# Kernel tuning notes

Measured on AMD Instinct MI355X. Metric: run time of the kernel, lower is better.

## Reference

```python
import jax, jax.numpy as jnp
import numpy as np

H = 2048      # hidden_size
F = 1408      # moe_intermediate_size
E = 8         # num_experts
K = 2         # num_activated_experts
B, S = 4, 1024


def setup_inputs() -> dict:
    key = jax.random.key(0)
    ks = jax.random.split(key, 9)
    sc = 0.02
    return {
        "hidden_states": jax.random.normal(ks[0], (B, S, H), dtype=jnp.float32),
        "gate_w": jax.random.normal(ks[1], (E, H), dtype=jnp.float32) * sc,
        "bias": jnp.zeros((E,), dtype=jnp.float32),
        # shared expert (num_shared_experts = 1); torch Linear weight layout [out, in]
        "ws1": jax.random.normal(ks[2], (F, H), dtype=jnp.float32) * sc,
        "ws2": jax.random.normal(ks[3], (H, F), dtype=jnp.float32) * sc,
        "ws3": jax.random.normal(ks[4], (F, H), dtype=jnp.float32) * sc,
        # routed experts stacked along leading E axis
        "we1": jax.random.normal(ks[5], (E, F, H), dtype=jnp.float32) * sc,
        "we2": jax.random.normal(ks[6], (E, H, F), dtype=jnp.float32) * sc,
        "we3": jax.random.normal(ks[7], (E, F, H), dtype=jnp.float32) * sc,
    }


def reference(hidden_states, gate_w, bias, ws1, ws2, ws3, we1, we2, we3):
    orig_shape = hidden_states.shape
    x = hidden_states.reshape(-1, orig_shape[-1])      # [T, H]
    T = x.shape[0]

    # shared expert (SwiGLU)
    shared = (jax.nn.silu(x @ ws1.T) * (x @ ws3.T)) @ ws2.T   # [T, H]

    # sigmoid gating with bias-adjusted top-k selection
    scores = jax.nn.sigmoid(x @ gate_w.T)              # [T, E]
    routing_scores = scores + bias
    _, topk_idx = jax.lax.top_k(routing_scores, K)     # [T, K]
    sel = jnp.take_along_axis(scores, topk_idx, axis=1)
    gates = sel / sel.sum(axis=-1, keepdims=True)      # [T, K]

    # dense combine weights c[t, e] (top-k indices are distinct per token)
    c = jnp.zeros((T, E), dtype=x.dtype).at[jnp.arange(T)[:, None], topk_idx].add(gates)

    # all-expert SwiGLU, combined with sparse gate weights
    h1 = jnp.einsum("th,efh->etf", x, we1)             # [E, T, F]
    h3 = jnp.einsum("th,efh->etf", x, we3)
    act = jax.nn.silu(h1) * h3
    routed = jnp.einsum("etf,ehf,te->th", act, we2, c) # [T, H]

    return (shared + routed).reshape(orig_shape)
```

## Files before the change

### kernel.cpp

```cpp
#include <hip/hip_runtime.h>
#include <cstdint>
#include <cstddef>

#define TDIM 4096
#define HDIM 2048
#define FDIM 1408
#define NEXP 8
#define NSLOT (TDIM * 2)
#define BK 32

typedef _Float16 half8 __attribute__((ext_vector_type(8)));
typedef _Float16 half4 __attribute__((ext_vector_type(4)));
typedef float floatx4 __attribute__((ext_vector_type(4)));

#define AS1 __attribute__((address_space(1)))
#define AS3 __attribute__((address_space(3)))

__device__ __forceinline__ void g2l16(const _Float16* g, _Float16* l) {
  __builtin_amdgcn_global_load_lds((const AS1 unsigned*)g, (AS3 unsigned*)l, 16, 0, 0);
}

static constexpr size_t ws_align(size_t x) { return (x + 511) & ~(size_t)511; }
static constexpr size_t WS_XB     = 0;
static constexpr size_t WS_ACT_S  = WS_XB    + (size_t)TDIM * HDIM * 2;
static constexpr size_t WS_ACT_R  = WS_ACT_S + (size_t)TDIM * FDIM * 2;
static constexpr size_t WS_TOKE   = WS_ACT_R + (size_t)NSLOT * FDIM * 2;
static constexpr size_t WS_TOKG   = WS_TOKE  + (size_t)TDIM * 2 * 4;
static constexpr size_t WS_SLOTT  = WS_TOKG  + (size_t)TDIM * 2 * 4;
static constexpr size_t WS_SLOTG  = WS_SLOTT + (size_t)NSLOT * 4;
static constexpr size_t WS_TOKS   = WS_SLOTG + (size_t)NSLOT * 4;
static constexpr size_t WS_COUNTS = WS_TOKS  + (size_t)TDIM * 2 * 4;
static constexpr size_t WS_FILL   = WS_COUNTS + 64;
static constexpr size_t WS_OFFS   = WS_FILL   + 64;
static constexpr size_t WS_WS1H   = ws_align(WS_OFFS + 64);
static constexpr size_t WS_WS3H   = WS_WS1H + (size_t)FDIM * HDIM * 2;
static constexpr size_t WS_WS2H   = WS_WS3H + (size_t)FDIM * HDIM * 2;
static constexpr size_t WS_WE1H   = WS_WS2H + (size_t)HDIM * FDIM * 2;
static constexpr size_t WS_WE3H   = WS_WE1H + (size_t)NEXP * FDIM * HDIM * 2;
static constexpr size_t WS_WE2H   = WS_WE3H + (size_t)NEXP * FDIM * HDIM * 2;
static constexpr size_t WS_H1S    = WS_WE2H + (size_t)NEXP * HDIM * FDIM * 2;
static constexpr size_t WS_H1R    = WS_H1S + (size_t)TDIM * FDIM * 2;
static constexpr size_t WS_RB     = WS_H1R + (size_t)NSLOT * FDIM * 2;
static constexpr size_t WS_END    = WS_RB + (size_t)NSLOT * HDIM * 2;


__global__ void zero_meta_kernel(int* __restrict__ counts) {
  if (threadIdx.x < 32) counts[threadIdx.x] = 0;
}

__global__ void cvt3_kernel(const float* __restrict__ s0, const float* __restrict__ s1,
                            const float* __restrict__ s2, _Float16* __restrict__ d0,
                            _Float16* __restrict__ d1, _Float16* __restrict__ d2) {
  const float* s;
  _Float16* d;
  if (blockIdx.y == 0)      { s = s0; d = d0; }
  else if (blockIdx.y == 1) { s = s1; d = d1; }
  else                      { s = s2; d = d2; }
  size_t i = ((size_t)blockIdx.x * 256 + threadIdx.x) * 8;
  float4 a = *(const float4*)(s + i);
  float4 b = *(const float4*)(s + i + 4);
  half8 h;
  h[0] = (_Float16)a.x; h[1] = (_Float16)a.y; h[2] = (_Float16)a.z; h[3] = (_Float16)a.w;
  h[4] = (_Float16)b.x; h[5] = (_Float16)b.y; h[6] = (_Float16)b.z; h[7] = (_Float16)b.w;
  *(half8*)(d + i) = h;
}

__global__ void gate_kernel(const float* __restrict__ x, const float* __restrict__ gw,
                            const float* __restrict__ bias, _Float16* __restrict__ xb,
                            int* __restrict__ toke, float* __restrict__ tokg,
                            int* __restrict__ counts) {
  const int wid  = blockIdx.x * 4 + (threadIdx.x >> 6);
  const int lane = threadIdx.x & 63;
  const float4* xv = (const float4*)(x + (size_t)wid * HDIM);
  const float4* gv = (const float4*)gw;
  _Float16* xrow = xb + (size_t)wid * HDIM;
  float acc[NEXP];
#pragma unroll
  for (int e = 0; e < NEXP; ++e) acc[e] = 0.f;
#pragma unroll
  for (int i = 0; i < 8; ++i) {
    float4 xq = xv[lane + 64 * i];
    half4 hq;
    hq[0] = (_Float16)xq.x; hq[1] = (_Float16)xq.y;
    hq[2] = (_Float16)xq.z; hq[3] = (_Float16)xq.w;
    *(half4*)(xrow + 4 * (lane + 64 * i)) = hq;
#pragma unroll
    for (int e = 0; e < NEXP; ++e) {
      float4 gq = gv[e * 512 + lane + 64 * i];
      acc[e] += xq.x * gq.x + xq.y * gq.y + xq.z * gq.z + xq.w * gq.w;
    }
  }
#pragma unroll
  for (int e = 0; e < NEXP; ++e) {
    float v = acc[e];
    for (int off = 32; off; off >>= 1) v += __shfl_xor(v, off);
    acc[e] = v;
  }
  if (lane == 0) {
    float s[NEXP], r[NEXP];
#pragma unroll
    for (int e = 0; e < NEXP; ++e) {
      s[e] = 1.f / (1.f + __expf(-acc[e]));
      r[e] = s[e] + bias[e];
    }
    int e0 = 0;
#pragma unroll
    for (int e = 1; e < NEXP; ++e) if (r[e] > r[e0]) e0 = e;
    int e1 = -1;
#pragma unroll
    for (int e = 0; e < NEXP; ++e) if (e != e0 && (e1 < 0 || r[e] > r[e1])) e1 = e;
    float g0 = s[e0], g1 = s[e1];
    float inv = 1.f / (g0 + g1);
    toke[wid * 2]     = e0;
    toke[wid * 2 + 1] = e1;
    tokg[wid * 2]     = g0 * inv;
    tokg[wid * 2 + 1] = g1 * inv;
    atomicAdd(&counts[e0], 1);
    atomicAdd(&counts[e1], 1);
  }
}

__global__ void offsets_kernel(const int* __restrict__ counts, int* __restrict__ offs) {
  if (threadIdx.x == 0) {
    int o = 0;
    for (int e = 0; e < NEXP; ++e) { offs[e] = o; o += counts[e]; }
  }
}

__global__ void scatter_kernel(const int* __restrict__ toke, const float* __restrict__ tokg,
                               const int* __restrict__ offs, int* __restrict__ fill,
                               int* __restrict__ slott, float* __restrict__ slotg,
                               int* __restrict__ tokslot) {
  int t = blockIdx.x * 256 + threadIdx.x;
#pragma unroll
  for (int j = 0; j < 2; ++j) {
    int e = toke[t * 2 + j];
    float g = tokg[t * 2 + j];
    int p = offs[e] + atomicAdd(&fill[e], 1);
    slott[p] = t;
    slotg[p] = g;
    tokslot[t * 2 + j] = p;
  }
}


template <bool FIN>
__global__ __launch_bounds__(256) void up_gemm(
    const _Float16* __restrict__ xb,
    const _Float16* __restrict__ wsh, const _Float16* __restrict__ weh,
    _Float16* __restrict__ dsts, _Float16* __restrict__ dstr,
    const _Float16* __restrict__ h1s, const _Float16* __restrict__ h1r,
    const int* __restrict__ counts, const int* __restrict__ offs,
    const int* __restrict__ slott) {
  constexpr int GX = FDIM / 128;
  constexpr int GY = TDIM / 128;
  const int orig = blockIdx.x + GX * (blockIdx.y + GY * blockIdx.z);
  const int k8 = orig & 7, s = orig >> 3;
  const int g = k8 + 8 * (s / GX);
  const int lid = g * GX + (s % GX);
  const int bx = lid % GX;
  const int by = (lid / GX) % GY;
  const int bz = lid / (GX * GY);

  int cnt = TDIM, base = 0;
  const _Float16* __restrict__ W = wsh;
  _Float16* __restrict__ dst = dsts;
  const _Float16* __restrict__ h1 = h1s;
  bool gather = false;
  if (bz > 0) {
    const int e = bz - 1;
    cnt = counts[e];
    base = offs[e];
    if ((int)(by * 128) >= cnt) return;
    W = weh + (size_t)e * FDIM * HDIM;
    dst = dstr;
    h1 = h1r;
    gather = true;
  }
  const int m0 = by * 128, n0 = bx * 128;

  __shared__ _Float16 As[2][128 * BK];
  __shared__ _Float16 Bs[2][128 * BK];

  const int tid = threadIdx.x, lane = tid & 63, wv = tid >> 6;
  const int wm = wv >> 1, wn = wv & 1;
  const int lrow = lane & 15, quad = lane >> 4;

  const _Float16 *srcA[2], *srcB[2];
#pragma unroll
  for (int j = 0; j < 2; ++j) {
    const int rr = wv * 32 + j * 16 + (lane >> 2);
    const int gc = ((lane & 3) ^ ((rr >> 1) & 3)) * 8;
    const int m = m0 + rr;
    int tok;
    if (gather) tok = slott[base + (m < cnt ? m : cnt - 1)];
    else tok = m;
    srcA[j] = xb + (size_t)tok * HDIM + gc;
    srcB[j] = W + (size_t)(n0 + rr) * HDIM + gc;
  }

  floatx4 acc[4][4] = {};
  const int cA = (quad ^ ((lrow >> 1) & 3)) * 8;

#pragma unroll
  for (int j = 0; j < 2; ++j) {
    const int lb = (wv * 32 + j * 16) * BK;
    g2l16(srcA[j], &As[0][lb]);
    g2l16(srcB[j], &Bs[0][lb]);
  }
  __syncthreads();

  for (int t = 0; t < HDIM / BK; ++t) {
    const int cur = t & 1;
    if (t + 1 < HDIM / BK) {
      const int k0 = (t + 1) * BK;
#pragma unroll
      for (int j = 0; j < 2; ++j) {
        const int lb = (wv * 32 + j * 16) * BK;
        g2l16(srcA[j] + k0, &As[cur ^ 1][lb]);
        g2l16(srcB[j] + k0, &Bs[cur ^ 1][lb]);
      }
    }
    half8 af[4], bf[4];
#pragma unroll
    for (int i = 0; i < 4; ++i)
      af[i] = *(const half8*)&As[cur][(wm * 64 + i * 16 + lrow) * BK + cA];
#pragma unroll
    for (int i = 0; i < 4; ++i)
      bf[i] = *(const half8*)&Bs[cur][(wn * 64 + i * 16 + lrow) * BK + cA];
#pragma unroll
    for (int ms = 0; ms < 4; ++ms)
#pragma unroll
      for (int ns = 0; ns < 4; ++ns)
        acc[ms][ns] = __builtin_amdgcn_mfma_f32_16x16x32_f16(af[ms], bf[ns], acc[ms][ns], 0, 0, 0);
    __syncthreads();
  }

#pragma unroll
  for (int ms = 0; ms < 4; ++ms)
#pragma unroll
    for (int ns = 0; ns < 4; ++ns)
#pragma unroll
      for (int r = 0; r < 4; ++r) {
        const int rl = wm * 64 + ms * 16 + quad * 4 + r;
        const int f = n0 + wn * 64 + ns * 16 + lrow;
        const int m = m0 + rl;
        if (gather && m >= cnt) continue;
        const size_t row = gather ? (size_t)(base + m) : (size_t)m;
        float v = acc[ms][ns][r];
        if constexpr (FIN) {
          float h = (float)h1[row * FDIM + f];
          float a = h / (1.f + __expf(-h)) * v;
          dst[row * FDIM + f] = (_Float16)a;
        } else {
          dst[row * FDIM + f] = (_Float16)v;
        }
      }
}

__global__ __launch_bounds__(256) void down_kernel(
    const _Float16* __restrict__ acts, const _Float16* __restrict__ actr,
    const _Float16* __restrict__ ws2h, const _Float16* __restrict__ we2h,
    float* __restrict__ out, _Float16* __restrict__ rbuf,
    const int* __restrict__ counts, const int* __restrict__ offs) {
  constexpr int GX = HDIM / 128;
  constexpr int GY = TDIM / 128;
  const int orig = blockIdx.x + GX * (blockIdx.y + GY * blockIdx.z);
  const int k8 = orig & 7, s = orig >> 3;
  const int g = k8 + 8 * (s / GX);
  const int lid = g * GX + (s % GX);
  const int bx = lid % GX;
  const int by = (lid / GX) % GY;
  const int bz = lid / (GX * GY);

  int cnt = TDIM, base = 0;
  const _Float16* __restrict__ A = acts;
  const _Float16* __restrict__ W = ws2h;
  bool gather = false;
  if (bz > 0) {
    const int e = bz - 1;
    cnt = counts[e];
    base = offs[e];
    if ((int)(by * 128) >= cnt) return;
    A = actr;
    W = we2h + (size_t)e * HDIM * FDIM;
    gather = true;
  }
  const int m0 = by * 128, n0 = bx * 128;

  __shared__ _Float16 As[2][128 * BK];
  __shared__ _Float16 Bs[2][128 * BK];

  const int tid = threadIdx.x, lane = tid & 63, wv = tid >> 6;
  const int wm = wv >> 1, wn = wv & 1;
  const int lrow = lane & 15, quad = lane >> 4;

  const _Float16 *srcA[2], *srcB[2];
#pragma unroll
  for (int j = 0; j < 2; ++j) {
    const int rr = wv * 32 + j * 16 + (lane >> 2);
    const int gc = ((lane & 3) ^ ((rr >> 1) & 3)) * 8;
    const int m = m0 + rr;
    int srow;
    if (gather) srow = base + (m < cnt ? m : cnt - 1);
    else srow = m;
    srcA[j] = A + (size_t)srow * FDIM + gc;
    srcB[j] = W + (size_t)(n0 + rr) * FDIM + gc;
  }

  floatx4 acc[4][4] = {};
  const int cA = (quad ^ ((lrow >> 1) & 3)) * 8;

#pragma unroll
  for (int j = 0; j < 2; ++j) {
    const int lb = (wv * 32 + j * 16) * BK;
    g2l16(srcA[j], &As[0][lb]);
    g2l16(srcB[j], &Bs[0][lb]);
  }
  __syncthreads();

  for (int t = 0; t < FDIM / BK; ++t) {
    const int cur = t & 1;
    if (t + 1 < FDIM / BK) {
      const int k0 = (t + 1) * BK;
#pragma unroll
      for (int j = 0; j < 2; ++j) {
        const int lb = (wv * 32 + j * 16) * BK;
        g2l16(srcA[j] + k0, &As[cur ^ 1][lb]);
        g2l16(srcB[j] + k0, &Bs[cur ^ 1][lb]);
      }
    }
    half8 af[4], bf[4];
#pragma unroll
    for (int i = 0; i < 4; ++i)
      af[i] = *(const half8*)&As[cur][(wm * 64 + i * 16 + lrow) * BK + cA];
#pragma unroll
    for (int i = 0; i < 4; ++i)
      bf[i] = *(const half8*)&Bs[cur][(wn * 64 + i * 16 + lrow) * BK + cA];
#pragma unroll
    for (int ms = 0; ms < 4; ++ms)
#pragma unroll
      for (int ns = 0; ns < 4; ++ns)
        acc[ms][ns] = __builtin_amdgcn_mfma_f32_16x16x32_f16(af[ms], bf[ns], acc[ms][ns], 0, 0, 0);
    __syncthreads();
  }

#pragma unroll
  for (int ms = 0; ms < 4; ++ms)
#pragma unroll
    for (int ns = 0; ns < 4; ++ns)
#pragma unroll
      for (int r = 0; r < 4; ++r) {
        float v = acc[ms][ns][r];
        const int rl = wm * 64 + ms * 16 + quad * 4 + r;
        const int h = n0 + wn * 64 + ns * 16 + lrow;
        const int m = m0 + rl;
        if (gather) {
          if (m < cnt) rbuf[(size_t)(base + m) * HDIM + h] = (_Float16)v;
        } else {
          out[(size_t)m * HDIM + h] = v;
        }
      }
}

__global__ void merge_kernel(float* __restrict__ out, const _Float16* __restrict__ rbuf,
                             const int* __restrict__ tokslot, const float* __restrict__ tokg) {
  const int t = blockIdx.x;
  const int hc = threadIdx.x * 8;
  const int p0 = tokslot[t * 2], p1 = tokslot[t * 2 + 1];
  const float g0 = tokg[t * 2], g1 = tokg[t * 2 + 1];
  half8 r0 = *(const half8*)(rbuf + (size_t)p0 * HDIM + hc);
  half8 r1 = *(const half8*)(rbuf + (size_t)p1 * HDIM + hc);
  float* o = out + (size_t)t * HDIM + hc;
  float4 a = *(float4*)o;
  float4 b = *(float4*)(o + 4);
  a.x += g0 * (float)r0[0] + g1 * (float)r1[0];
  a.y += g0 * (float)r0[1] + g1 * (float)r1[1];
  a.z += g0 * (float)r0[2] + g1 * (float)r1[2];
  a.w += g0 * (float)r0[3] + g1 * (float)r1[3];
  b.x += g0 * (float)r0[4] + g1 * (float)r1[4];
  b.y += g0 * (float)r0[5] + g1 * (float)r1[5];
  b.z += g0 * (float)r0[6] + g1 * (float)r1[6];
  b.w += g0 * (float)r0[7] + g1 * (float)r1[7];
  *(float4*)o = a;
  *(float4*)(o + 4) = b;
}


extern "C" void kernel_launch(void* const* d_in, const int* in_sizes, int n_in,
                              void* d_out, int out_size, void* d_ws, size_t ws_size,
                              hipStream_t stream) {
  const float* x    = (const float*)d_in[0];
  const float* gw   = (const float*)d_in[1];
  const float* bias = (const float*)d_in[2];
  const float* ws1  = (const float*)d_in[3];
  const float* ws2  = (const float*)d_in[4];
  const float* ws3  = (const float*)d_in[5];
  const float* we1  = (const float*)d_in[6];
  const float* we2  = (const float*)d_in[7];
  const float* we3  = (const float*)d_in[8];
  float* out = (float*)d_out;

  char* ws = (char*)d_ws;
  _Float16* xb   = (_Float16*)(ws + WS_XB);
  _Float16* acts = (_Float16*)(ws + WS_ACT_S);
  _Float16* actr = (_Float16*)(ws + WS_ACT_R);
  int*   toke  = (int*)(ws + WS_TOKE);
  float* tokg  = (float*)(ws + WS_TOKG);
  int*   slott = (int*)(ws + WS_SLOTT);
  float* slotg = (float*)(ws + WS_SLOTG);
  int*   toks  = (int*)(ws + WS_TOKS);
  int* counts  = (int*)(ws + WS_COUNTS);
  int* fill    = (int*)(ws + WS_FILL);
  int* offs    = (int*)(ws + WS_OFFS);
  _Float16* ws1h = (_Float16*)(ws + WS_WS1H);
  _Float16* ws3h = (_Float16*)(ws + WS_WS3H);
  _Float16* ws2h = (_Float16*)(ws + WS_WS2H);
  _Float16* we1h = (_Float16*)(ws + WS_WE1H);
  _Float16* we3h = (_Float16*)(ws + WS_WE3H);
  _Float16* we2h = (_Float16*)(ws + WS_WE2H);
  _Float16* h1s  = (_Float16*)(ws + WS_H1S);
  _Float16* h1r  = (_Float16*)(ws + WS_H1R);
  _Float16* rbuf = (_Float16*)(ws + WS_RB);

  hipLaunchKernelGGL(zero_meta_kernel, dim3(1), dim3(64), 0, stream, counts);
  hipLaunchKernelGGL(gate_kernel, dim3(1024), dim3(256), 0, stream, x, gw, bias, xb, toke, tokg, counts);
  hipLaunchKernelGGL(offsets_kernel, dim3(1), dim3(64), 0, stream, counts, offs);
  hipLaunchKernelGGL(scatter_kernel, dim3(16), dim3(256), 0, stream, toke, tokg, offs, fill, slott, slotg, toks);

  constexpr int GS = (FDIM * HDIM) / 2048;
  constexpr int GR = (NEXP * FDIM * HDIM) / 2048;
  hipLaunchKernelGGL(cvt3_kernel, dim3(GS, 3), dim3(256), 0, stream, ws1, ws3, ws2, ws1h, ws3h, ws2h);
  hipLaunchKernelGGL(cvt3_kernel, dim3(GR, 3), dim3(256), 0, stream, we1, we3, we2, we1h, we3h, we2h);

  hipLaunchKernelGGL((up_gemm<false>), dim3(FDIM / 128, TDIM / 128, NEXP + 1), dim3(256), 0, stream,
                     xb, ws1h, we1h, h1s, h1r, nullptr, nullptr, counts, offs, slott);
  hipLaunchKernelGGL((up_gemm<true>), dim3(FDIM / 128, TDIM / 128, NEXP + 1), dim3(256), 0, stream,
                     xb, ws3h, we3h, acts, actr, h1s, h1r, counts, offs, slott);
  hipLaunchKernelGGL(down_kernel, dim3(HDIM / 128, TDIM / 128, NEXP + 1), dim3(256), 0, stream,
                     acts, actr, ws2h, we2h, out, rbuf, counts, offs);
  hipLaunchKernelGGL(merge_kernel, dim3(TDIM), dim3(256), 0, stream, out, rbuf, toks, tokg);
}
```

Before: 912.8 us.

## Double K-tile depth and drop LDS double buffering in expert GEMMs

Raises the K tile from 32 to 64 in both expert GEMM kernels and replaces the ping-pong LDS buffers with one buffer that is filled, synchronised, consumed in two 32-wide MFMA steps, then synchronised again. The LDS swizzle is rewritten to an 8-chunk XOR pattern to match the 128-byte rows. The aim is to halve the K-loop trip count and barrier overhead per unit of work at the same LDS footprint. In exchange, the next tile's global-to-LDS loads no longer overlap with MFMA work, so memory latency is exposed inside each block unless other resident blocks hide it.

Result: slower. 954.6 us (+4.6%).

```diff
diff --git a/kernel.cpp b/kernel.cpp
--- a/kernel.cpp
+++ b/kernel.cpp
@@ -7,7 +7,7 @@
 #define FDIM 1408
 #define NEXP 8
 #define NSLOT (TDIM * 2)
-#define BK 32
+#define BK 64
 
 typedef _Float16 half8 __attribute__((ext_vector_type(8)));
 typedef _Float16 half4 __attribute__((ext_vector_type(4)));
@@ -179,60 +179,54 @@
   }
   const int m0 = by * 128, n0 = bx * 128;
 
-  __shared__ _Float16 As[2][128 * BK];
-  __shared__ _Float16 Bs[2][128 * BK];
+  __shared__ _Float16 As[128 * BK];
+  __shared__ _Float16 Bs[128 * BK];
 
   const int tid = threadIdx.x, lane = tid & 63, wv = tid >> 6;
   const int wm = wv >> 1, wn = wv & 1;
   const int lrow = lane & 15, quad = lane >> 4;
 
-  const _Float16 *srcA[2], *srcB[2];
-#pragma unroll
-  for (int j = 0; j < 2; ++j) {
-    const int rr = wv * 32 + j * 16 + (lane >> 2);
-    const int gc = ((lane & 3) ^ ((rr >> 1) & 3)) * 8;
+  const _Float16 *srcA[4], *srcB[4];
+  int lb_[4];
+#pragma unroll
+  for (int j = 0; j < 4; ++j) {
+    const int rr = wv * 32 + j * 8 + (lane >> 3);
+    const int gc = ((lane & 7) ^ (lane >> 3)) * 8;
     const int m = m0 + rr;
     int tok;
     if (gather) tok = slott[base + (m < cnt ? m : cnt - 1)];
     else tok = m;
     srcA[j] = xb + (size_t)tok * HDIM + gc;
     srcB[j] = W + (size_t)(n0 + rr) * HDIM + gc;
+    lb_[j] = (wv * 32 + j * 8) * BK;
   }
 
   floatx4 acc[4][4] = {};
-  const int cA = (quad ^ ((lrow >> 1) & 3)) * 8;
-
-#pragma unroll
-  for (int j = 0; j < 2; ++j) {
-    const int lb = (wv * 32 + j * 16) * BK;
-    g2l16(srcA[j], &As[0][lb]);
-    g2l16(srcB[j], &Bs[0][lb]);
-  }
-  __syncthreads();
 
   for (int t = 0; t < HDIM / BK; ++t) {
-    const int cur = t & 1;
-    if (t + 1 < HDIM / BK) {
-      const int k0 = (t + 1) * BK;
-#pragma unroll
-      for (int j = 0; j < 2; ++j) {
-        const int lb = (wv * 32 + j * 16) * BK;
-        g2l16(srcA[j] + k0, &As[cur ^ 1][lb]);
-        g2l16(srcB[j] + k0, &Bs[cur ^ 1][lb]);
-      }
-    }
-    half8 af[4], bf[4];
-#pragma unroll
-    for (int i = 0; i < 4; ++i)
-      af[i] = *(const half8*)&As[cur][(wm * 64 + i * 16 + lrow) * BK + cA];
-#pragma unroll
-    for (int i = 0; i < 4; ++i)
-      bf[i] = *(const half8*)&Bs[cur][(wn * 64 + i * 16 + lrow) * BK + cA];
-#pragma unroll
-    for (int ms = 0; ms < 4; ++ms)
-#pragma unroll
-      for (int ns = 0; ns < 4; ++ns)
-        acc[ms][ns] = __builtin_amdgcn_mfma_f32_16x16x32_f16(af[ms], bf[ns], acc[ms][ns], 0, 0, 0);
+    const int k0 = t * BK;
+#pragma unroll
+    for (int j = 0; j < 4; ++j) {
+      g2l16(srcA[j] + k0, &As[lb_[j]]);
+      g2l16(srcB[j] + k0, &Bs[lb_[j]]);
+    }
+    __syncthreads();
+#pragma unroll
+    for (int kk = 0; kk < BK; kk += 32) {
+      const int co = ((((kk >> 3) + quad) ^ (lrow & 7))) * 8;
+      half8 af[4], bf[4];
+#pragma unroll
+      for (int i = 0; i < 4; ++i)
+        af[i] = *(const half8*)&As[(wm * 64 + i * 16 + lrow) * BK + co];
+#pragma unroll
+      for (int i = 0; i < 4; ++i)
+        bf[i] = *(const half8*)&Bs[(wn * 64 + i * 16 + lrow) * BK + co];
+#pragma unroll
+      for (int ms = 0; ms < 4; ++ms)
+#pragma unroll
+        for (int ns = 0; ns < 4; ++ns)
+          acc[ms][ns] = __builtin_amdgcn_mfma_f32_16x16x32_f16(af[ms], bf[ns], acc[ms][ns], 0, 0, 0);
+    }
     __syncthreads();
   }
 
@@ -288,60 +282,54 @@
   }
   const int m0 = by * 128, n0 = bx * 128;
 
-  __shared__ _Float16 As[2][128 * BK];
-  __shared__ _Float16 Bs[2][128 * BK];
+  __shared__ _Float16 As[128 * BK];
+  __shared__ _Float16 Bs[128 * BK];
 
   const int tid = threadIdx.x, lane = tid & 63, wv = tid >> 6;
   const int wm = wv >> 1, wn = wv & 1;
   const int lrow = lane & 15, quad = lane >> 4;
 
-  const _Float16 *srcA[2], *srcB[2];
-#pragma unroll
-  for (int j = 0; j < 2; ++j) {
-    const int rr = wv * 32 + j * 16 + (lane >> 2);
-    const int gc = ((lane & 3) ^ ((rr >> 1) & 3)) * 8;
+  const _Float16 *srcA[4], *srcB[4];
+  int lb_[4];
+#pragma unroll
+  for (int j = 0; j < 4; ++j) {
+    const int rr = wv * 32 + j * 8 + (lane >> 3);
+    const int gc = ((lane & 7) ^ (lane >> 3)) * 8;
     const int m = m0 + rr;
     int srow;
     if (gather) srow = base + (m < cnt ? m : cnt - 1);
     else srow = m;
     srcA[j] = A + (size_t)srow * FDIM + gc;
     srcB[j] = W + (size_t)(n0 + rr) * FDIM + gc;
+    lb_[j] = (wv * 32 + j * 8) * BK;
   }
 
   floatx4 acc[4][4] = {};
-  const int cA = (quad ^ ((lrow >> 1) & 3)) * 8;
-
-#pragma unroll
-  for (int j = 0; j < 2; ++j) {
-    const int lb = (wv * 32 + j * 16) * BK;
-    g2l16(srcA[j], &As[0][lb]);
-    g2l16(srcB[j], &Bs[0][lb]);
-  }
-  __syncthreads();
 
   for (int t = 0; t < FDIM / BK; ++t) {
-    const int cur = t & 1;
-    if (t + 1 < FDIM / BK) {
-      const int k0 = (t + 1) * BK;
-#pragma unroll
-      for (int j = 0; j < 2; ++j) {
-        const int lb = (wv * 32 + j * 16) * BK;
-        g2l16(srcA[j] + k0, &As[cur ^ 1][lb]);
-        g2l16(srcB[j] + k0, &Bs[cur ^ 1][lb]);
-      }
-    }
-    half8 af[4], bf[4];
-#pragma unroll
-    for (int i = 0; i < 4; ++i)
-      af[i] = *(const half8*)&As[cur][(wm * 64 + i * 16 + lrow) * BK + cA];
-#pragma unroll
-    for (int i = 0; i < 4; ++i)
-      bf[i] = *(const half8*)&Bs[cur][(wn * 64 + i * 16 + lrow) * BK + cA];
-#pragma unroll
-    for (int ms = 0; ms < 4; ++ms)
-#pragma unroll
-      for (int ns = 0; ns < 4; ++ns)
-        acc[ms][ns] = __builtin_amdgcn_mfma_f32_16x16x32_f16(af[ms], bf[ns], acc[ms][ns], 0, 0, 0);
+    const int k0 = t * BK;
+#pragma unroll
+    for (int j = 0; j < 4; ++j) {
+      g2l16(srcA[j] + k0, &As[lb_[j]]);
+      g2l16(srcB[j] + k0, &Bs[lb_[j]]);
+    }
+    __syncthreads();
+#pragma unroll
+    for (int kk = 0; kk < BK; kk += 32) {
+      const int co = ((((kk >> 3) + quad) ^ (lrow & 7))) * 8;
+      half8 af[4], bf[4];
+#pragma unroll
+      for (int i = 0; i < 4; ++i)
+        af[i] = *(const half8*)&As[(wm * 64 + i * 16 + lrow) * BK + co];
+#pragma unroll
+      for (int i = 0; i < 4; ++i)
+        bf[i] = *(const half8*)&Bs[(wn * 64 + i * 16 + lrow) * BK + co];
+#pragma unroll
+      for (int ms = 0; ms < 4; ++ms)
+#pragma unroll
+        for (int ns = 0; ns < 4; ++ns)
+          acc[ms][ns] = __builtin_amdgcn_mfma_f32_16x16x32_f16(af[ms], bf[ns], acc[ms][ns], 0, 0, 0);
+    }
     __syncthreads();
   }
 
```
